# Optimization experiments

Hardware: AMD Instinct MI355X
Metric: run time of the kernel (lower is better)

The kernel has to match this reference:

```python
import jax, jax.numpy as jnp
import numpy as np

N_SPK, N_UTT, D = 1024, 32, 128
EPS = 1e-8  # matches F.cosine_similarity eps


def setup_inputs() -> dict:
    key = jax.random.key(0)
    emb = jax.random.normal(key, (N_SPK * N_UTT, D), dtype=jnp.float32)
    emb = emb / jnp.linalg.norm(emb, axis=-1, keepdims=True)  # L2-normalized per docstring
    return {
        "embeddings": emb,
        "w": jnp.asarray(10.0, dtype=jnp.float32),
        "b": jnp.asarray(-5.0, dtype=jnp.float32),
        "n_speakers": N_SPK,
        "n_utterances": N_UTT,
    }


def reference(embeddings, w, b, n_speakers, n_utterances):
    # [N, M, D]
    e = embeddings.reshape(n_speakers, n_utterances, -1)
    cent = e.mean(axis=1)  # [N, D] full centroids
    # exclusive centroids: mean over all utterances except i -> [N, M, D]
    cent_excl = (e.sum(axis=1, keepdims=True) - e) / (n_utterances - 1)

    e_n = jnp.maximum(jnp.linalg.norm(e, axis=-1), EPS)          # [N, M]
    c_n = jnp.maximum(jnp.linalg.norm(cent, axis=-1), EPS)       # [N]
    ce_n = jnp.maximum(jnp.linalg.norm(cent_excl, axis=-1), EPS) # [N, M]

    # cosine sim of every utterance vs every full centroid: [N, M, N]
    sim = jnp.einsum('nmd,kd->nmk', e, cent) / (e_n[:, :, None] * c_n[None, None, :])
    # own-speaker entry uses the exclusive centroid instead
    sim_own = jnp.sum(e * cent_excl, axis=-1) / (e_n * ce_n)     # [N, M]
    eye = jnp.eye(n_speakers, dtype=bool)[:, None, :]            # [N, 1, N]
    sim = jnp.where(eye, sim_own[:, :, None], sim)

    logits = (w * sim + b).reshape(n_speakers * n_utterances, n_speakers)
    targets = jnp.repeat(jnp.arange(n_speakers), n_utterances)
    logp = jax.nn.log_softmax(logits, axis=-1)
    loss = -jnp.take_along_axis(logp, targets[:, None], axis=-1).mean()
    return loss
```

## Files before the change

### kernel.cpp

```cpp
#include <hip/hip_runtime.h>
#include <math.h>

#define NSPK 1024
#define NUTT 32
#define DIM  128
#define NROWS (NSPK * NUTT)
#define EPS 1e-8f
#define LOG2E 1.44269504f

typedef __attribute__((ext_vector_type(8))) short short8;
typedef __attribute__((ext_vector_type(4))) float floatx4;

__device__ inline unsigned short f2bf(float f) {
  union { float f; unsigned u; } v; v.f = f;
  unsigned r = v.u + 0x7fffu + ((v.u >> 16) & 1u);
  return (unsigned short)(r >> 16);
}

__global__ __launch_bounds__(256) void k_prep(const float* __restrict__ emb,
                                              const float* __restrict__ wp,
                                              const float* __restrict__ bp,
                                              unsigned short* __restrict__ centN,
                                              float* __restrict__ rs2,
                                              float* __restrict__ eol,
                                              float* __restrict__ olv) {
  __shared__ __align__(16) float E[32 * 132];
  __shared__ __align__(16) float Sl[128];
  __shared__ float red2[2];

  int n = blockIdx.x, t = threadIdx.x;

  const float4* e4 = (const float4*)emb + (size_t)n * 1024;
#pragma unroll
  for (int i = 0; i < 4; ++i) {
    int idx4 = t + 256 * i;
    int m = idx4 >> 5, d4 = (idx4 & 31) << 2;
    *(float4*)&E[m * 132 + d4] = e4[idx4];
  }
  __syncthreads();

  float s = 0.f;
  if (t < 128) {
    for (int m = 0; m < 32; ++m) s += E[m * 132 + t];
    Sl[t] = s;
    float p = s * s;
#pragma unroll
    for (int mask = 1; mask < 64; mask <<= 1) p += __shfl_xor(p, mask, 64);
    if ((t & 63) == 0) red2[t >> 6] = p;
  }
  __syncthreads();
  float ss = red2[0] + red2[1];

  if (t < 128) {
    float cn = fmaxf(sqrtf(ss) * (1.0f / NUTT), EPS);
    centN[(size_t)n * DIM + t] = f2bf(s / (NUTT * cn));
  }

  int row = t >> 3, sub = t & 7;
  float ee = 0.f, es = 0.f;
  int base = row * 132 + sub * 16;
#pragma unroll
  for (int i = 0; i < 4; ++i) {
    float4 ev = *(const float4*)&E[base + i * 4];
    float4 sv = *(const float4*)&Sl[sub * 16 + i * 4];
    ee += ev.x * ev.x + ev.y * ev.y + ev.z * ev.z + ev.w * ev.w;
    es += ev.x * sv.x + ev.y * sv.y + ev.z * sv.z + ev.w * sv.w;
  }
#pragma unroll
  for (int mask = 1; mask < 8; mask <<= 1) {
    ee += __shfl_xor(ee, mask, 64);
    es += __shfl_xor(es, mask, 64);
  }
  if (sub == 0) {
    float w = wp[0], b = bp[0];
    float M = b + fabsf(w);
    float en = fmaxf(sqrtf(ee), EPS);
    float dot_own = (es - ee) * (1.0f / (NUTT - 1));
    float ex2 = (ss - 2.0f * es + ee) * (1.0f / ((NUTT - 1) * (NUTT - 1)));
    float cen = fmaxf(sqrtf(ex2), EPS);
    float ol = w * dot_own / (en * cen) + b;
    int r = n * NUTT + row;
    olv[r] = ol;
    eol[r] = exp2f((ol - M) * LOG2E);
    rs2[r] = w * LOG2E / en;
  }
}

__global__ __launch_bounds__(256, 2) void k_mfma(const float* __restrict__ emb,
                                                 const unsigned short* __restrict__ centN,
                                                 const float* __restrict__ rs2g,
                                                 const float* __restrict__ eolg,
                                                 const float* __restrict__ olvg,
                                                 const float* __restrict__ wp,
                                                 const float* __restrict__ bp,
                                                 float* __restrict__ out) {
  __shared__ __align__(16) unsigned short A[64 * 136];
  __shared__ float sPart[4 * 64];

  int b = blockIdx.x, t = threadIdx.x;
  int wid = t >> 6, lane = t & 63;
  int lg = lane >> 4, lc = lane & 15;
  int s0 = b * 2;

  const float4* e4 = (const float4*)emb + (size_t)b * 2048;
#pragma unroll
  for (int i = 0; i < 8; ++i) {
    int idx4 = t + 256 * i;
    int lr = idx4 >> 5, d4 = (idx4 & 31) << 2;
    float4 v = e4[idx4];
    ushort4 bv;
    bv.x = f2bf(v.x); bv.y = f2bf(v.y); bv.z = f2bf(v.z); bv.w = f2bf(v.w);
    *(ushort4*)&A[lr * 136 + d4] = bv;
  }
  __syncthreads();

  short8 af[4][4];
#pragma unroll
  for (int rt = 0; rt < 4; ++rt)
#pragma unroll
    for (int ks = 0; ks < 4; ++ks)
      af[rt][ks] = *(const short8*)&A[(rt * 16 + lc) * 136 + ks * 32 + lg * 8];

  float rsL[16], eolL[16];
#pragma unroll
  for (int rt = 0; rt < 4; ++rt) {
    float4 r4 = *(const float4*)&rs2g[b * 64 + rt * 16 + lg * 4];
    float4 o4 = *(const float4*)&eolg[b * 64 + rt * 16 + lg * 4];
    rsL[rt * 4 + 0] = r4.x; rsL[rt * 4 + 1] = r4.y; rsL[rt * 4 + 2] = r4.z; rsL[rt * 4 + 3] = r4.w;
    eolL[rt * 4 + 0] = o4.x; eolL[rt * 4 + 1] = o4.y; eolL[rt * 4 + 2] = o4.z; eolL[rt * 4 + 3] = o4.w;
  }

  float w = wp[0], bb = bp[0];
  float M = bb + fabsf(w);
  float c2 = (bb - M) * LOG2E;

  float sAcc[16];
#pragma unroll
  for (int j = 0; j < 16; ++j) sAcc[j] = 0.f;

  int colbase = wid * 256;
#pragma unroll 2
  for (int ct = 0; ct < 16; ++ct) {
    int c0 = colbase + ct * 16;
    int col = c0 + lc;
    const short8* bptr = (const short8*)(centN + (size_t)col * DIM + lg * 8);
    short8 bf[4];
#pragma unroll
    for (int ks = 0; ks < 4; ++ks) bf[ks] = bptr[ks * 4];

    floatx4 acc[4];
#pragma unroll
    for (int rt = 0; rt < 4; ++rt) acc[rt] = (floatx4){0.f, 0.f, 0.f, 0.f};
#pragma unroll
    for (int ks = 0; ks < 4; ++ks)
#pragma unroll
      for (int rt = 0; rt < 4; ++rt)
        acc[rt] = __builtin_amdgcn_mfma_f32_16x16x32_bf16(af[rt][ks], bf[ks], acc[rt], 0, 0, 0);

    bool fix = (unsigned)(s0 - c0) < 16u;
#pragma unroll
    for (int rt = 0; rt < 4; ++rt) {
      int own = s0 + (rt >> 1);
#pragma unroll
      for (int reg = 0; reg < 4; ++reg) {
        float l2 = fmaf(rsL[rt * 4 + reg], acc[rt][reg], c2);
        float e = exp2f(l2);
        if (fix && col == own) e = eolL[rt * 4 + reg];
        sAcc[rt * 4 + reg] += e;
      }
    }
  }

#pragma unroll
  for (int mask = 1; mask < 16; mask <<= 1)
#pragma unroll
    for (int j = 0; j < 16; ++j) sAcc[j] += __shfl_xor(sAcc[j], mask, 64);

  if (lc == 0)
#pragma unroll
    for (int rt = 0; rt < 4; ++rt)
#pragma unroll
      for (int reg = 0; reg < 4; ++reg)
        sPart[wid * 64 + rt * 16 + lg * 4 + reg] = sAcc[rt * 4 + reg];
  __syncthreads();

  if (t < 64) {
    float st = sPart[t] + sPart[64 + t] + sPart[128 + t] + sPart[192 + t];
    float lossr = M + logf(st) - olvg[b * 64 + t];
#pragma unroll
    for (int mask = 1; mask < 64; mask <<= 1) lossr += __shfl_xor(lossr, mask, 64);
    if (t == 0) atomicAdd(out, lossr * (1.0f / NROWS));
  }
}

extern "C" void kernel_launch(void* const* d_in, const int* in_sizes, int n_in,
                              void* d_out, int out_size, void* d_ws, size_t ws_size,
                              hipStream_t stream) {
  const float* emb = (const float*)d_in[0];
  const float* wp  = (const float*)d_in[1];
  const float* bp  = (const float*)d_in[2];

  char* ws = (char*)d_ws;
  unsigned short* centN = (unsigned short*)ws;
  float* rs2 = (float*)(ws + 262144);
  float* eol = (float*)(ws + 262144 + 131072);
  float* olv = (float*)(ws + 262144 + 262144);
  float* out = (float*)d_out;

  hipMemsetAsync(d_out, 0, sizeof(float), stream);
  hipLaunchKernelGGL(k_prep, dim3(NSPK), dim3(256), 0, stream,
                     emb, wp, bp, centN, rs2, eol, olv);
  hipLaunchKernelGGL(k_mfma, dim3(NSPK / 2), dim3(256), 0, stream,
                     emb, centN, rs2, eol, olv, wp, bp, out);
}
```

Measured before the change: 98.25 us.

## Restructure prep and MFMA kernels with wider blocks and B-fragment prefetch

The prep kernel now handles two speakers per block, reads embeddings straight from global memory instead of staging them in LDS, and zeroes the output itself, which removes the separate memset. The MFMA kernel uses 512-thread blocks, so each wave covers 32 rows rather than 64, and it double-buffers the centroid B-fragments to prefetch the next column tile. The goal is higher occupancy, more latency hiding and one fewer launch. Having block 0 of k1 zero the output relies on stream ordering between k1 and k2, and the prep kernel's global reads are less coalesced.

```diff
diff --git a/kernel.cpp b/kernel.cpp
--- a/kernel.cpp
+++ b/kernel.cpp
@@ -17,150 +17,153 @@
   return (unsigned short)(r >> 16);
 }
 
-__global__ __launch_bounds__(256) void k_prep(const float* __restrict__ emb,
-                                              const float* __restrict__ wp,
-                                              const float* __restrict__ bp,
-                                              unsigned short* __restrict__ centN,
-                                              float* __restrict__ rs2,
-                                              float* __restrict__ eol,
-                                              float* __restrict__ olv) {
-  __shared__ __align__(16) float E[32 * 132];
-  __shared__ __align__(16) float Sl[128];
-  __shared__ float red2[2];
-
-  int n = blockIdx.x, t = threadIdx.x;
-
-  const float4* e4 = (const float4*)emb + (size_t)n * 1024;
+__global__ __launch_bounds__(256) void k1(const float* __restrict__ emb,
+                                          const float* __restrict__ wp,
+                                          const float* __restrict__ bp,
+                                          unsigned short* __restrict__ centN,
+                                          float* __restrict__ rs2g,
+                                          float* __restrict__ eolg,
+                                          float* __restrict__ olvg,
+                                          float* __restrict__ out) {
+  __shared__ __align__(16) float Sl[2 * 128];
+  __shared__ float red[4];
+
+  int b = blockIdx.x, t = threadIdx.x;
+  float w = wp[0], bb = bp[0];
+  float M = bb + fabsf(w);
+  if (b == 0 && t == 0) out[0] = 0.f;
+
+  int sp = t >> 7, d = t & 127;
+  {
+    const float* eb = emb + (size_t)(b * 2 + sp) * NUTT * DIM + d;
+    float s = 0.f;
+#pragma unroll
+    for (int m = 0; m < NUTT; ++m) s += eb[m * DIM];
+    Sl[sp * 128 + d] = s;
+    float p = s * s;
+#pragma unroll
+    for (int mask = 1; mask < 64; mask <<= 1) p += __shfl_xor(p, mask, 64);
+    if ((t & 63) == 0) red[t >> 6] = p;
+  }
+  __syncthreads();
+  float ss0 = red[0] + red[1], ss1 = red[2] + red[3];
+
+  {
+    float ss = sp ? ss1 : ss0;
+    float s = Sl[sp * 128 + d];
+    float cn = fmaxf(sqrtf(ss) * (1.0f / NUTT), EPS);
+    centN[(size_t)(b * 2 + sp) * DIM + d] = f2bf(s / (NUTT * cn));
+  }
+
+  {
+    int row = t >> 2, sub = t & 3;
+    int rsp = row >> 5;
+    const float* er = emb + (size_t)(b * 64 + row) * DIM + sub * 32;
+    const float* Srow = &Sl[rsp * 128 + sub * 32];
+    float ee = 0.f, es = 0.f;
+#pragma unroll
+    for (int i = 0; i < 8; ++i) {
+      float4 ev = *(const float4*)&er[i * 4];
+      float4 sv = *(const float4*)&Srow[i * 4];
+      ee += ev.x * ev.x + ev.y * ev.y + ev.z * ev.z + ev.w * ev.w;
+      es += ev.x * sv.x + ev.y * sv.y + ev.z * sv.z + ev.w * sv.w;
+    }
+    ee += __shfl_xor(ee, 1, 64); es += __shfl_xor(es, 1, 64);
+    ee += __shfl_xor(ee, 2, 64); es += __shfl_xor(es, 2, 64);
+    if (sub == 0) {
+      float ss = rsp ? ss1 : ss0;
+      float en = fmaxf(sqrtf(ee), EPS);
+      float dot_own = (es - ee) * (1.0f / (NUTT - 1));
+      float ex2 = (ss - 2.f * es + ee) * (1.0f / ((NUTT - 1) * (NUTT - 1)));
+      float cen = fmaxf(sqrtf(ex2), EPS);
+      float ol = w * dot_own / (en * cen) + bb;
+      int gr = b * 64 + row;
+      olvg[gr] = ol;
+      eolg[gr] = exp2f((ol - M) * LOG2E);
+      rs2g[gr] = w * LOG2E / en;
+    }
+  }
+}
+
+__global__ __launch_bounds__(512, 4) void k2(const float* __restrict__ emb,
+                                             const unsigned short* __restrict__ centN,
+                                             const float* __restrict__ rs2g,
+                                             const float* __restrict__ eolg,
+                                             const float* __restrict__ olvg,
+                                             const float* __restrict__ wp,
+                                             const float* __restrict__ bp,
+                                             float* __restrict__ out) {
+  __shared__ __align__(16) unsigned short A[64 * 136];
+  __shared__ __align__(16) float sPart[256];
+
+  int b = blockIdx.x, t = threadIdx.x;
+  float w = wp[0], bb = bp[0];
+  float M = bb + fabsf(w);
+  float c2 = -fabsf(w) * LOG2E;
+
 #pragma unroll
   for (int i = 0; i < 4; ++i) {
-    int idx4 = t + 256 * i;
-    int m = idx4 >> 5, d4 = (idx4 & 31) << 2;
-    *(float4*)&E[m * 132 + d4] = e4[idx4];
-  }
-  __syncthreads();
-
-  float s = 0.f;
-  if (t < 128) {
-    for (int m = 0; m < 32; ++m) s += E[m * 132 + t];
-    Sl[t] = s;
-    float p = s * s;
-#pragma unroll
-    for (int mask = 1; mask < 64; mask <<= 1) p += __shfl_xor(p, mask, 64);
-    if ((t & 63) == 0) red2[t >> 6] = p;
-  }
-  __syncthreads();
-  float ss = red2[0] + red2[1];
-
-  if (t < 128) {
-    float cn = fmaxf(sqrtf(ss) * (1.0f / NUTT), EPS);
-    centN[(size_t)n * DIM + t] = f2bf(s / (NUTT * cn));
-  }
-
-  int row = t >> 3, sub = t & 7;
-  float ee = 0.f, es = 0.f;
-  int base = row * 132 + sub * 16;
-#pragma unroll
-  for (int i = 0; i < 4; ++i) {
-    float4 ev = *(const float4*)&E[base + i * 4];
-    float4 sv = *(const float4*)&Sl[sub * 16 + i * 4];
-    ee += ev.x * ev.x + ev.y * ev.y + ev.z * ev.z + ev.w * ev.w;
-    es += ev.x * sv.x + ev.y * sv.y + ev.z * sv.z + ev.w * sv.w;
-  }
-#pragma unroll
-  for (int mask = 1; mask < 8; mask <<= 1) {
-    ee += __shfl_xor(ee, mask, 64);
-    es += __shfl_xor(es, mask, 64);
-  }
-  if (sub == 0) {
-    float w = wp[0], b = bp[0];
-    float M = b + fabsf(w);
-    float en = fmaxf(sqrtf(ee), EPS);
-    float dot_own = (es - ee) * (1.0f / (NUTT - 1));
-    float ex2 = (ss - 2.0f * es + ee) * (1.0f / ((NUTT - 1) * (NUTT - 1)));
-    float cen = fmaxf(sqrtf(ex2), EPS);
-    float ol = w * dot_own / (en * cen) + b;
-    int r = n * NUTT + row;
-    olv[r] = ol;
-    eol[r] = exp2f((ol - M) * LOG2E);
-    rs2[r] = w * LOG2E / en;
-  }
-}
-
-__global__ __launch_bounds__(256, 2) void k_mfma(const float* __restrict__ emb,
-                                                 const unsigned short* __restrict__ centN,
-                                                 const float* __restrict__ rs2g,
-                                                 const float* __restrict__ eolg,
-                                                 const float* __restrict__ olvg,
-                                                 const float* __restrict__ wp,
-                                                 const float* __restrict__ bp,
-                                                 float* __restrict__ out) {
-  __shared__ __align__(16) unsigned short A[64 * 136];
-  __shared__ float sPart[4 * 64];
-
-  int b = blockIdx.x, t = threadIdx.x;
-  int wid = t >> 6, lane = t & 63;
-  int lg = lane >> 4, lc = lane & 15;
-  int s0 = b * 2;
-
-  const float4* e4 = (const float4*)emb + (size_t)b * 2048;
-#pragma unroll
-  for (int i = 0; i < 8; ++i) {
-    int idx4 = t + 256 * i;
-    int lr = idx4 >> 5, d4 = (idx4 & 31) << 2;
-    float4 v = e4[idx4];
+    int idx4 = t + 512 * i;
+    int r = idx4 >> 5, d4 = (idx4 & 31) << 2;
+    float4 v = *(const float4*)(emb + (size_t)b * 8192 + (size_t)idx4 * 4);
     ushort4 bv;
     bv.x = f2bf(v.x); bv.y = f2bf(v.y); bv.z = f2bf(v.z); bv.w = f2bf(v.w);
-    *(ushort4*)&A[lr * 136 + d4] = bv;
+    *(ushort4*)&A[r * 136 + d4] = bv;
   }
   __syncthreads();
 
-  short8 af[4][4];
-#pragma unroll
-  for (int rt = 0; rt < 4; ++rt)
+  int wid = t >> 6, lane = t & 63, lg = lane >> 4, lc = lane & 15;
+  int h = wid >> 2, q = wid & 3;
+  int own = b * 2 + h;
+
+  short8 af[2][4];
+#pragma unroll
+  for (int rt = 0; rt < 2; ++rt)
 #pragma unroll
     for (int ks = 0; ks < 4; ++ks)
-      af[rt][ks] = *(const short8*)&A[(rt * 16 + lc) * 136 + ks * 32 + lg * 8];
-
-  float rsL[16], eolL[16];
-#pragma unroll
-  for (int rt = 0; rt < 4; ++rt) {
-    float4 r4 = *(const float4*)&rs2g[b * 64 + rt * 16 + lg * 4];
-    float4 o4 = *(const float4*)&eolg[b * 64 + rt * 16 + lg * 4];
+      af[rt][ks] = *(const short8*)&A[(h * 32 + rt * 16 + lc) * 136 + ks * 32 + lg * 8];
+
+  float rsL[8], eolL[8];
+#pragma unroll
+  for (int rt = 0; rt < 2; ++rt) {
+    float4 r4 = *(const float4*)&rs2g[b * 64 + h * 32 + rt * 16 + lg * 4];
+    float4 o4 = *(const float4*)&eolg[b * 64 + h * 32 + rt * 16 + lg * 4];
     rsL[rt * 4 + 0] = r4.x; rsL[rt * 4 + 1] = r4.y; rsL[rt * 4 + 2] = r4.z; rsL[rt * 4 + 3] = r4.w;
     eolL[rt * 4 + 0] = o4.x; eolL[rt * 4 + 1] = o4.y; eolL[rt * 4 + 2] = o4.z; eolL[rt * 4 + 3] = o4.w;
   }
 
-  float w = wp[0], bb = bp[0];
-  float M = bb + fabsf(w);
-  float c2 = (bb - M) * LOG2E;
-
-  float sAcc[16];
-#pragma unroll
-  for (int j = 0; j < 16; ++j) sAcc[j] = 0.f;
-
-  int colbase = wid * 256;
-#pragma unroll 2
+  float sAcc[8];
+#pragma unroll
+  for (int j = 0; j < 8; ++j) sAcc[j] = 0.f;
+
+  int colbase = q * 256;
+  int col0 = colbase + lc;
+  const short8* cb8 = (const short8*)centN;
+
+  short8 bcur[4], bnxt[4];
+  {
+    const short8* p = cb8 + (size_t)col0 * 16 + lg;
+    bcur[0] = p[0]; bcur[1] = p[4]; bcur[2] = p[8]; bcur[3] = p[12];
+  }
+
   for (int ct = 0; ct < 16; ++ct) {
-    int c0 = colbase + ct * 16;
-    int col = c0 + lc;
-    const short8* bptr = (const short8*)(centN + (size_t)col * DIM + lg * 8);
-    short8 bf[4];
-#pragma unroll
-    for (int ks = 0; ks < 4; ++ks) bf[ks] = bptr[ks * 4];
-
-    floatx4 acc[4];
-#pragma unroll
-    for (int rt = 0; rt < 4; ++rt) acc[rt] = (floatx4){0.f, 0.f, 0.f, 0.f};
+    if (ct < 15) {
+      const short8* p = cb8 + (size_t)(col0 + (ct + 1) * 16) * 16 + lg;
+      bnxt[0] = p[0]; bnxt[1] = p[4]; bnxt[2] = p[8]; bnxt[3] = p[12];
+    }
+    floatx4 acc[2];
+#pragma unroll
+    for (int rt = 0; rt < 2; ++rt) acc[rt] = (floatx4){0.f, 0.f, 0.f, 0.f};
 #pragma unroll
     for (int ks = 0; ks < 4; ++ks)
 #pragma unroll
-      for (int rt = 0; rt < 4; ++rt)
-        acc[rt] = __builtin_amdgcn_mfma_f32_16x16x32_bf16(af[rt][ks], bf[ks], acc[rt], 0, 0, 0);
-
-    bool fix = (unsigned)(s0 - c0) < 16u;
-#pragma unroll
-    for (int rt = 0; rt < 4; ++rt) {
-      int own = s0 + (rt >> 1);
+      for (int rt = 0; rt < 2; ++rt)
+        acc[rt] = __builtin_amdgcn_mfma_f32_16x16x32_bf16(af[rt][ks], bcur[ks], acc[rt], 0, 0, 0);
+
+    int c0 = colbase + ct * 16, col = c0 + lc;
+    bool fix = (unsigned)(own - c0) < 16u;
+#pragma unroll
+    for (int rt = 0; rt < 2; ++rt)
 #pragma unroll
       for (int reg = 0; reg < 4; ++reg) {
         float l2 = fmaf(rsL[rt * 4 + reg], acc[rt][reg], c2);
@@ -168,24 +171,27 @@
         if (fix && col == own) e = eolL[rt * 4 + reg];
         sAcc[rt * 4 + reg] += e;
       }
-    }
+#pragma unroll
+    for (int ks = 0; ks < 4; ++ks) bcur[ks] = bnxt[ks];
   }
 
 #pragma unroll
   for (int mask = 1; mask < 16; mask <<= 1)
 #pragma unroll
-    for (int j = 0; j < 16; ++j) sAcc[j] += __shfl_xor(sAcc[j], mask, 64);
+    for (int j = 0; j < 8; ++j) sAcc[j] += __shfl_xor(sAcc[j], mask, 64);
 
   if (lc == 0)
 #pragma unroll
-    for (int rt = 0; rt < 4; ++rt)
+    for (int rt = 0; rt < 2; ++rt)
 #pragma unroll
       for (int reg = 0; reg < 4; ++reg)
-        sPart[wid * 64 + rt * 16 + lg * 4 + reg] = sAcc[rt * 4 + reg];
+        sPart[wid * 32 + rt * 16 + lg * 4 + reg] = sAcc[rt * 4 + reg];
   __syncthreads();
 
   if (t < 64) {
-    float st = sPart[t] + sPart[64 + t] + sPart[128 + t] + sPart[192 + t];
+    int hh = t >> 5, ri = t & 31;
+    float st = sPart[(hh * 4 + 0) * 32 + ri] + sPart[(hh * 4 + 1) * 32 + ri] +
+               sPart[(hh * 4 + 2) * 32 + ri] + sPart[(hh * 4 + 3) * 32 + ri];
     float lossr = M + logf(st) - olvg[b * 64 + t];
 #pragma unroll
     for (int mask = 1; mask < 64; mask <<= 1) lossr += __shfl_xor(lossr, mask, 64);
@@ -202,14 +208,13 @@
 
   char* ws = (char*)d_ws;
   unsigned short* centN = (unsigned short*)ws;
-  float* rs2 = (float*)(ws + 262144);
-  float* eol = (float*)(ws + 262144 + 131072);
-  float* olv = (float*)(ws + 262144 + 262144);
+  float* rs2g = (float*)(ws + 262144);
+  float* eolg = (float*)(ws + 262144 + 131072);
+  float* olvg = (float*)(ws + 262144 + 262144);
   float* out = (float*)d_out;
 
-  hipMemsetAsync(d_out, 0, sizeof(float), stream);
-  hipLaunchKernelGGL(k_prep, dim3(NSPK), dim3(256), 0, stream,
-                     emb, wp, bp, centN, rs2, eol, olv);
-  hipLaunchKernelGGL(k_mfma, dim3(NSPK / 2), dim3(256), 0, stream,
-                     emb, centN, rs2, eol, olv, wp, bp, out);
-}
+  hipLaunchKernelGGL(k1, dim3(512), dim3(256), 0, stream,
+                     emb, wp, bp, centN, rs2g, eolg, olvg, out);
+  hipLaunchKernelGGL(k2, dim3(512), dim3(512), 0, stream,
+                     emb, centN, rs2g, eolg, olvg, wp, bp, out);
+}
```

After: 161.5 us. 64.4% more time.
